# Kernel tuning notes

Hardware: AMD Instinct MI355X
Metric: run time of the kernel (lower is better)

Reference implementation:

```python
import jax, jax.numpy as jnp
import numpy as np

N_NODES = 100000
N_EDGES = 1600000
IN_F = 64
OUT_F = 32
NEG_SLOPE = 0.2


def setup_inputs() -> dict:
    key = jax.random.key(0)
    k = jax.random.split(key, 6)
    x = jax.random.normal(k[0], (N_NODES, IN_F), dtype=jnp.float32)
    edge_index = jax.random.randint(k[1], (2, N_EDGES), 0, N_NODES, dtype=jnp.int64)
    W = jax.random.normal(k[2], (IN_F, OUT_F), dtype=jnp.float32) * 0.1
    att_src = jax.random.normal(k[3], (OUT_F,), dtype=jnp.float32) * 0.1
    att_dst = jax.random.normal(k[4], (OUT_F,), dtype=jnp.float32) * 0.1
    bias = jax.random.normal(k[5], (OUT_F,), dtype=jnp.float32) * 0.1
    return {"x": x, "edge_index": edge_index, "W": W,
            "att_src": att_src, "att_dst": att_dst, "bias": bias}


def reference(x, edge_index, W, att_src, att_dst, bias):
    N = x.shape[0]
    # Linear projection (single head, concat=True -> [N, OUT_F])
    h = x @ W  # [N, C]
    a_src = h @ att_src  # [N] per-node source attention logit contribution
    a_dst = h @ att_dst  # [N] per-node destination contribution
    # add self loops (PyG GATConv default add_self_loops=True)
    loop = jnp.arange(N, dtype=edge_index.dtype)
    src = jnp.concatenate([edge_index[0], loop])  # [E+N] message senders
    dst = jnp.concatenate([edge_index[1], loop])  # [E+N] message receivers
    # attention logits per edge, LeakyReLU(alpha_src[j] + alpha_dst[i])
    e = jax.nn.leaky_relu(a_src[src] + a_dst[dst], NEG_SLOPE)
    # segment softmax over incoming edges of each destination node
    m = jax.ops.segment_max(e, dst, num_segments=N)  # every node has a self loop
    ex = jnp.exp(e - m[dst])
    denom = jax.ops.segment_sum(ex, dst, num_segments=N)
    alpha = ex / denom[dst]  # [E+N]
    # weighted scatter-add of source features into destinations
    out = jax.ops.segment_sum(h[src] * alpha[:, None], dst, num_segments=N)
    out = out + bias
    # GATLayer activation='relu'
    return jax.nn.relu(out)
```

## Files before the change

kernel.cpp:

```cpp
#include <hip/hip_runtime.h>
#include <hip/hip_fp16.h>
#include <math.h>

#define IN_F 64
#define OUT_F 32
#define NEG_SLOPE 0.2f

#define BK_SHIFT 7
#define BK 128
#define NBMAX 1024
#define NBLKA 256
#define PSTAGE 10
#define PADSLACK (BK * 15)

typedef _Float16 half8_t __attribute__((ext_vector_type(8)));
typedef float float4_t __attribute__((ext_vector_type(4)));
typedef int int4_t __attribute__((ext_vector_type(4)));


__device__ __forceinline__ float leaky(float v) {
    return (v > 0.0f) ? v : NEG_SLOPE * v;
}

__device__ __forceinline__ int incScan256(int v, int tid, int* wsum) {
    const int lane = tid & 63, wid = tid >> 6;
    #pragma unroll
    for (int m = 1; m < 64; m <<= 1) {
        int u = __shfl_up(v, m);
        if (lane >= m) v += u;
    }
    if (lane == 63) wsum[wid] = v;
    __syncthreads();
    int add = 0;
    for (int k = 0; k < wid; ++k) add += wsum[k];
    __syncthreads();
    return v + add;
}

__device__ __forceinline__ int incScan512(int v, int tid, int* wsum) {
    const int lane = tid & 63, wid = tid >> 6;
    #pragma unroll
    for (int m = 1; m < 64; m <<= 1) {
        int u = __shfl_up(v, m);
        if (lane >= m) v += u;
    }
    if (lane == 63) wsum[wid] = v;
    __syncthreads();
    int add = 0;
    for (int k = 0; k < wid; ++k) add += wsum[k];
    __syncthreads();
    return v + add;
}

__global__ __launch_bounds__(256) void k_projhist(
        const float* __restrict__ x, const float* __restrict__ W,
        const float* __restrict__ att_src, const float* __restrict__ att_dst,
        __half2* __restrict__ h2, float* __restrict__ asrc, float* __restrict__ adst,
        const int* __restrict__ dst, int* __restrict__ hist,
        int N, int NB, int E, int epb, int PB) {
    __shared__ int smem[2560];
    const int tid = threadIdx.x;

    if (blockIdx.x >= PB) {
        int* lh = smem;
        const int blk = blockIdx.x - PB;
        for (int i = tid; i < NB; i += 256) lh[i] = 0;
        __syncthreads();
        const int e0 = blk * epb, e1 = min(E, e0 + epb);
        for (int e = e0 + tid; e < e1; e += 256) atomicAdd(&lh[dst[e] >> BK_SHIFT], 1);
        __syncthreads();
        for (int b = tid; b < NB; b += 256) hist[(size_t)b * NBLKA + blk] = lh[b];
        return;
    }

    const int wv   = tid >> 6;
    const int lane = tid & 63;
    const int m    = lane & 15;
    const int quad = lane >> 4;
    const int node0 = (blockIdx.x * 4 + wv) * 16;
    if (node0 >= N) return;

    const int kb = quad * 8;
    half8_t b00, b01, b10, b11;
    #pragma unroll
    for (int j = 0; j < 8; ++j) {
        b00[j] = (_Float16)W[(kb + j) * OUT_F + m];
        b01[j] = (_Float16)W[(32 + kb + j) * OUT_F + m];
        b10[j] = (_Float16)W[(kb + j) * OUT_F + 16 + m];
        b11[j] = (_Float16)W[(32 + kb + j) * OUT_F + 16 + m];
    }
    const int row = min(node0 + m, N - 1);
    const float* xr = x + (size_t)row * IN_F + kb;
    float4_t xa = *(const float4_t*)(xr);
    float4_t xb = *(const float4_t*)(xr + 4);
    float4_t xc = *(const float4_t*)(xr + 32);
    float4_t xd = *(const float4_t*)(xr + 36);
    half8_t a0, a1;
    #pragma unroll
    for (int j = 0; j < 4; ++j) {
        a0[j] = (_Float16)xa[j]; a0[4 + j] = (_Float16)xb[j];
        a1[j] = (_Float16)xc[j]; a1[4 + j] = (_Float16)xd[j];
    }
    float4_t acc0 = {0.f, 0.f, 0.f, 0.f};
    float4_t acc1 = {0.f, 0.f, 0.f, 0.f};
    acc0 = __builtin_amdgcn_mfma_f32_16x16x32_f16(a0, b00, acc0, 0, 0, 0);
    acc0 = __builtin_amdgcn_mfma_f32_16x16x32_f16(a1, b01, acc0, 0, 0, 0);
    acc1 = __builtin_amdgcn_mfma_f32_16x16x32_f16(a0, b10, acc1, 0, 0, 0);
    acc1 = __builtin_amdgcn_mfma_f32_16x16x32_f16(a1, b11, acc1, 0, 0, 0);

    const float aS0 = att_src[m], aS1 = att_src[16 + m];
    const float aD0 = att_dst[m], aD1 = att_dst[16 + m];
    #pragma unroll
    for (int r = 0; r < 4; ++r) {
        const int node = node0 + quad * 4 + r;
        float h0 = acc0[r], h1 = acc1[r];
        float h0p = __shfl_xor(h0, 1);
        float h1p = __shfl_xor(h1, 1);
        if (node < N && (m & 1) == 0) {
            __half2 hv;
            hv.x = __float2half_rn(h0); hv.y = __float2half_rn(h0p);
            h2[(size_t)node * 16 + (m >> 1)] = hv;
            __half2 hw;
            hw.x = __float2half_rn(h1); hw.y = __float2half_rn(h1p);
            h2[(size_t)node * 16 + 8 + (m >> 1)] = hw;
        }
        float vs = h0 * aS0 + h1 * aS1;
        float vd = h0 * aD0 + h1 * aD1;
        #pragma unroll
        for (int mm = 1; mm < 16; mm <<= 1) {
            vs += __shfl_xor(vs, mm);
            vd += __shfl_xor(vd, mm);
        }
        if (node < N && m == 0) {
            asrc[node] = vs;
            adst[node] = vd;
        }
    }
}

__global__ __launch_bounds__(256) void k_scan1(int* __restrict__ hist,
                                               int* __restrict__ bsum,
                                               __half2* __restrict__ h2,
                                               float* __restrict__ asrc,
                                               int N, int NB) {
    __shared__ int wsum[4];
    const int b = blockIdx.x, tid = threadIdx.x;
    if (b == 0) {
        if (tid < 16) h2[(size_t)N * 16 + tid] = __floats2half2_rn(0.0f, 0.0f);
        if (tid == 16) asrc[N] = -1e30f;
    }
    int v = hist[(size_t)b * NBLKA + tid];
    const int inc = incScan256(v, tid, wsum);
    hist[(size_t)b * NBLKA + tid] = inc - v;
    if (tid == 255) bsum[b] = inc;
}

__global__ __launch_bounds__(512) void k_bpart(const int* __restrict__ src,
                                               const int* __restrict__ dst,
                                               const int* __restrict__ hist,
                                               const int* __restrict__ bsum,
                                               int* __restrict__ recs,
                                               int NB, int E, int epb) {
    __shared__ int tt[NBMAX];
    __shared__ int lcur[NBMAX];
    __shared__ int wsum[8];
    const int tid = threadIdx.x, blk = blockIdx.x;
    for (int i = tid; i < NBMAX; i += 512) tt[i] = (i < NB) ? bsum[i] : 0;
    __syncthreads();
    {
        int a0 = tt[tid * 2], a1 = tt[tid * 2 + 1];
        int s = a0 + a1;
        int inc = incScan512(s, tid, wsum);
        int run = inc - s;
        tt[tid * 2] = run; run += a0;
        tt[tid * 2 + 1] = run;
    }
    __syncthreads();
    for (int b = tid; b < NB; b += 512)
        lcur[b] = hist[(size_t)b * NBLKA + blk] + tt[b];
    __syncthreads();
    const int e0 = blk * epb, e1 = min(E, e0 + epb);
    for (int e = e0 + tid; e < e1; e += 512) {
        int s = src[e];
        int d = dst[e];
        int p = atomicAdd(&lcur[d >> BK_SHIFT], 1);
        recs[p] = ((d & (BK - 1)) << 17) | s;
    }
}

__global__ __launch_bounds__(256) void k_place(const int* __restrict__ recs,
                                               const int* __restrict__ bsum,
                                               int* __restrict__ cnt,
                                               int* __restrict__ offs,
                                               int* __restrict__ col,
                                               int NB, int E, int N) {
    __shared__ int tt[NBMAX];
    __shared__ int fineCnt[BK];
    __shared__ int cur[BK];
    __shared__ int wsum[4];
    const int b = blockIdx.x, tid = threadIdx.x;
    for (int i = tid; i < NBMAX; i += 256) tt[i] = (i < NB) ? bsum[i] : 0;
    __syncthreads();
    {
        int a0 = tt[tid * 4], a1 = tt[tid * 4 + 1], a2 = tt[tid * 4 + 2], a3 = tt[tid * 4 + 3];
        int s = a0 + a1 + a2 + a3;
        int inc = incScan256(s, tid, wsum);
        int run = inc - s;
        tt[tid * 4] = run;     run += a0;
        tt[tid * 4 + 1] = run; run += a1;
        tt[tid * 4 + 2] = run; run += a2;
        tt[tid * 4 + 3] = run;
    }
    __syncthreads();
    const int cb0 = tt[b];
    const int cb1 = (b + 1 < NB) ? tt[b + 1] : E;
    const int count = cb1 - cb0;
    const int colBase = cb0 + b * PADSLACK;
    for (int i = tid; i < count + PADSLACK; i += 256) col[colBase + i] = N;
    int myrec[PSTAGE];
    if (tid < BK) fineCnt[tid] = 0;
    __syncthreads();
    #pragma unroll
    for (int k = 0; k < PSTAGE; ++k) {
        int i = tid + k * 256;
        if (i < count) {
            int v = recs[cb0 + i];
            myrec[k] = v;
            atomicAdd(&fineCnt[v >> 17], 1);
        }
    }
    for (int i = tid + PSTAGE * 256; i < count; i += 256)
        atomicAdd(&fineCnt[recs[cb0 + i] >> 17], 1);
    __syncthreads();
    const int v0 = (tid < BK) ? fineCnt[tid] : 0;
    const int pv = (v0 + 15) & ~15;
    const int pinc = incScan256(pv, tid, wsum);
    const int pexcl = pinc - pv;
    if (tid < BK) {
        const int node = (b << BK_SHIFT) + tid;
        if (node < N) {
            cnt[node]  = pv;
            offs[node] = colBase + pexcl;
        }
        cur[tid] = colBase + pexcl;
    }
    __syncthreads();
    #pragma unroll
    for (int k = 0; k < PSTAGE; ++k) {
        int i = tid + k * 256;
        if (i < count) {
            int r = myrec[k];
            int p = atomicAdd(&cur[r >> 17], 1);
            col[p] = r & 0x1FFFF;
        }
    }
    for (int i = tid + PSTAGE * 256; i < count; i += 256) {
        int r = recs[cb0 + i];
        int p = atomicAdd(&cur[r >> 17], 1);
        col[p] = r & 0x1FFFF;
    }
}

__global__ void k_gather(const int* __restrict__ col, const int* __restrict__ offs,
                         const int* __restrict__ cnt, const float* __restrict__ asrc,
                         const float* __restrict__ adst, const __half2* __restrict__ h2,
                         const float* __restrict__ bias, float* __restrict__ out, int N) {
    int t = blockIdx.x * 256 + threadIdx.x;
    int n = t >> 6;
    if (n >= N) return;
    const int lane = t & 63;
    const int g  = lane >> 4;
    const int c2 = lane & 15;
    const float adst_n = adst[n];
    float l = 0.0f, accx = 0.0f, accy = 0.0f;
    if (g == 0) {
        float p = __expf(leaky(asrc[n] + adst_n));
        float2 hv = __half22float2(h2[(size_t)n * 16 + c2]);
        l = p; accx = p * hv.x; accy = p * hv.y;
    }
    const int off = offs[n];
    const int q = cnt[n] >> 2;
    const int j0 = off + g * q;
    const int jend = j0 + q;
    for (int j = j0; j < jend; j += 4) {
        int s0 = col[j], s1 = col[j + 1], s2 = col[j + 2], s3 = col[j + 3];
        float a0 = asrc[s0], a1 = asrc[s1], a2 = asrc[s2], a3 = asrc[s3];
        float2 h0 = __half22float2(h2[(size_t)s0 * 16 + c2]);
        float2 h1 = __half22float2(h2[(size_t)s1 * 16 + c2]);
        float2 hv2 = __half22float2(h2[(size_t)s2 * 16 + c2]);
        float2 h3 = __half22float2(h2[(size_t)s3 * 16 + c2]);
        float p0 = __expf(leaky(a0 + adst_n));
        float p1 = __expf(leaky(a1 + adst_n));
        float p2 = __expf(leaky(a2 + adst_n));
        float p3 = __expf(leaky(a3 + adst_n));
        l += (p0 + p1) + (p2 + p3);
        accx += p0 * h0.x + p1 * h1.x + p2 * hv2.x + p3 * h3.x;
        accy += p0 * h0.y + p1 * h1.y + p2 * hv2.y + p3 * h3.y;
    }
    l    += __shfl_xor(l, 16);    l    += __shfl_xor(l, 32);
    accx += __shfl_xor(accx, 16); accx += __shfl_xor(accx, 32);
    accy += __shfl_xor(accy, 16); accy += __shfl_xor(accy, 32);
    if (g == 0) {
        float inv = 1.0f / l;
        float2 bb = ((const float2*)bias)[c2];
        float2 o;
        o.x = fmaxf(accx * inv + bb.x, 0.0f);
        o.y = fmaxf(accy * inv + bb.y, 0.0f);
        ((float2*)out)[(size_t)n * 16 + c2] = o;
    }
}

extern "C" void kernel_launch(void* const* d_in, const int* in_sizes, int n_in,
                              void* d_out, int out_size, void* d_ws, size_t ws_size,
                              hipStream_t stream) {
    const float* x        = (const float*)d_in[0];
    const int*   eidx     = (const int*)d_in[1];
    const float* W        = (const float*)d_in[2];
    const float* att_src  = (const float*)d_in[3];
    const float* att_dst  = (const float*)d_in[4];
    const float* bias     = (const float*)d_in[5];
    float* out = (float*)d_out;

    const int N = in_sizes[0] / IN_F;
    const int E = in_sizes[1] / 2;
    const int* src = eidx;
    const int* dst = eidx + E;

    const int NB  = (N + BK - 1) >> BK_SHIFT;
    const int epb = (E + NBLKA - 1) / NBLKA;

    int* u = (int*)d_ws;
    size_t o = 0;
    __half2* h2   = (__half2*)(u + o); o += (size_t)(N + 1) * 16;
    float*   asrc = (float*)(u + o);   o += N + 1;
    float*   adst = (float*)(u + o);   o += N;
    int*     cnt  = u + o;             o += N;
    int*     offs = u + o;             o += N;
    int*     hist = u + o;             o += (size_t)NB * NBLKA;
    int*     bsum = u + o;             o += NBMAX;
    int*     col  = u + o;             o += (size_t)E + (size_t)NB * PADSLACK;
    int*     recs = u + o;             o += E;

    const int PB = (N + 63) / 64;
    const int gatherBlocks = ((size_t)N * 64 + 255) / 256;

    k_projhist<<<PB + NBLKA, 256, 0, stream>>>(x, W, att_src, att_dst, h2, asrc, adst,
                                               dst, hist, N, NB, E, epb, PB);
    k_scan1<<<NB, 256, 0, stream>>>(hist, bsum, h2, asrc, N, NB);
    k_bpart<<<NBLKA, 512, 0, stream>>>(src, dst, hist, bsum, recs, NB, E, epb);
    k_place<<<NB, 256, 0, stream>>>(recs, bsum, cnt, offs, col, NB, E, N);
    k_gather<<<gatherBlocks, 256, 0, stream>>>(col, offs, cnt, asrc, adst, h2, bias, out, N);
}
```

Before: 175.0 us.

## Fuse CSR placement and gather into one kernel with LDS-resident column lists

Merges the k_place and k_gather kernels. Each 128-node bucket block now sorts its edge records into a shared-memory column array and computes its nodes' softmax-weighted aggregation directly from LDS. This removes the global col/offs/cnt writes and reads, one kernel launch, and the larger 16-entry per-node padding, which is now 4. The trade-offs are a fixed LDS capacity of 4096 entries per bucket that fails on skewed graphs, and only NB blocks of 512 threads doing the gather, which may reduce parallelism compared with one wavefront per node.

```diff
diff --git a/kernel.cpp b/kernel.cpp
--- a/kernel.cpp
+++ b/kernel.cpp
@@ -10,8 +10,8 @@
 #define BK 128
 #define NBMAX 1024
 #define NBLKA 256
-#define PSTAGE 10
-#define PADSLACK (BK * 15)
+#define PSTAGE 5
+#define COLCAP 4096
 
 typedef _Float16 half8_t __attribute__((ext_vector_type(8)));
 typedef float float4_t __attribute__((ext_vector_type(4)));
@@ -188,125 +188,129 @@
     }
 }
 
-__global__ __launch_bounds__(256) void k_place(const int* __restrict__ recs,
-                                               const int* __restrict__ bsum,
-                                               int* __restrict__ cnt,
-                                               int* __restrict__ offs,
-                                               int* __restrict__ col,
-                                               int NB, int E, int N) {
+__global__ __launch_bounds__(512) void k_pg(const int* __restrict__ recs,
+                                            const int* __restrict__ bsum,
+                                            const float* __restrict__ asrc,
+                                            const float* __restrict__ adst,
+                                            const __half2* __restrict__ h2,
+                                            const float* __restrict__ bias,
+                                            float* __restrict__ out,
+                                            int NB, int E, int N) {
     __shared__ int tt[NBMAX];
+    __shared__ __align__(16) int colsh[COLCAP];
     __shared__ int fineCnt[BK];
     __shared__ int cur[BK];
-    __shared__ int wsum[4];
+    __shared__ int loff[BK];
+    __shared__ int lpad[BK];
+    __shared__ int wsum[8];
     const int b = blockIdx.x, tid = threadIdx.x;
-    for (int i = tid; i < NBMAX; i += 256) tt[i] = (i < NB) ? bsum[i] : 0;
+    const int node0 = b << BK_SHIFT;
+
+    for (int i = tid; i < NBMAX; i += 512) tt[i] = (i < NB) ? bsum[i] : 0;
     __syncthreads();
     {
-        int a0 = tt[tid * 4], a1 = tt[tid * 4 + 1], a2 = tt[tid * 4 + 2], a3 = tt[tid * 4 + 3];
-        int s = a0 + a1 + a2 + a3;
-        int inc = incScan256(s, tid, wsum);
+        int a0 = tt[tid * 2], a1 = tt[tid * 2 + 1];
+        int s = a0 + a1;
+        int inc = incScan512(s, tid, wsum);
         int run = inc - s;
-        tt[tid * 4] = run;     run += a0;
-        tt[tid * 4 + 1] = run; run += a1;
-        tt[tid * 4 + 2] = run; run += a2;
-        tt[tid * 4 + 3] = run;
+        tt[tid * 2] = run;
+        tt[tid * 2 + 1] = run + a0;
     }
     __syncthreads();
     const int cb0 = tt[b];
     const int cb1 = (b + 1 < NB) ? tt[b + 1] : E;
     const int count = cb1 - cb0;
-    const int colBase = cb0 + b * PADSLACK;
-    for (int i = tid; i < count + PADSLACK; i += 256) col[colBase + i] = N;
+
+    for (int i = tid; i < COLCAP; i += 512) colsh[i] = N;
+    if (tid < BK) fineCnt[tid] = 0;
+    __syncthreads();
+
     int myrec[PSTAGE];
-    if (tid < BK) fineCnt[tid] = 0;
-    __syncthreads();
     #pragma unroll
     for (int k = 0; k < PSTAGE; ++k) {
-        int i = tid + k * 256;
+        int i = tid + k * 512;
         if (i < count) {
             int v = recs[cb0 + i];
             myrec[k] = v;
             atomicAdd(&fineCnt[v >> 17], 1);
         }
     }
-    for (int i = tid + PSTAGE * 256; i < count; i += 256)
+    for (int i = tid + PSTAGE * 512; i < count; i += 512)
         atomicAdd(&fineCnt[recs[cb0 + i] >> 17], 1);
     __syncthreads();
+
     const int v0 = (tid < BK) ? fineCnt[tid] : 0;
-    const int pv = (v0 + 15) & ~15;
-    const int pinc = incScan256(pv, tid, wsum);
-    const int pexcl = pinc - pv;
+    const int pv = (v0 + 3) & ~3;
+    const int vin = (tid < BK) ? pv : 0;
+    const int pinc = incScan512(vin, tid, wsum);
+    const int pexcl = pinc - vin;
     if (tid < BK) {
-        const int node = (b << BK_SHIFT) + tid;
-        if (node < N) {
-            cnt[node]  = pv;
-            offs[node] = colBase + pexcl;
-        }
-        cur[tid] = colBase + pexcl;
-    }
-    __syncthreads();
+        loff[tid] = pexcl;
+        lpad[tid] = pv;
+        cur[tid]  = pexcl;
+    }
+    __syncthreads();
+
     #pragma unroll
     for (int k = 0; k < PSTAGE; ++k) {
-        int i = tid + k * 256;
+        int i = tid + k * 512;
         if (i < count) {
             int r = myrec[k];
             int p = atomicAdd(&cur[r >> 17], 1);
-            col[p] = r & 0x1FFFF;
-        }
-    }
-    for (int i = tid + PSTAGE * 256; i < count; i += 256) {
+            colsh[p] = r & 0x1FFFF;
+        }
+    }
+    for (int i = tid + PSTAGE * 512; i < count; i += 512) {
         int r = recs[cb0 + i];
         int p = atomicAdd(&cur[r >> 17], 1);
-        col[p] = r & 0x1FFFF;
-    }
-}
-
-__global__ void k_gather(const int* __restrict__ col, const int* __restrict__ offs,
-                         const int* __restrict__ cnt, const float* __restrict__ asrc,
-                         const float* __restrict__ adst, const __half2* __restrict__ h2,
-                         const float* __restrict__ bias, float* __restrict__ out, int N) {
-    int t = blockIdx.x * 256 + threadIdx.x;
-    int n = t >> 6;
-    if (n >= N) return;
-    const int lane = t & 63;
-    const int g  = lane >> 4;
-    const int c2 = lane & 15;
-    const float adst_n = adst[n];
-    float l = 0.0f, accx = 0.0f, accy = 0.0f;
-    if (g == 0) {
-        float p = __expf(leaky(asrc[n] + adst_n));
-        float2 hv = __half22float2(h2[(size_t)n * 16 + c2]);
-        l = p; accx = p * hv.x; accy = p * hv.y;
-    }
-    const int off = offs[n];
-    const int q = cnt[n] >> 2;
-    const int j0 = off + g * q;
-    const int jend = j0 + q;
-    for (int j = j0; j < jend; j += 4) {
-        int s0 = col[j], s1 = col[j + 1], s2 = col[j + 2], s3 = col[j + 3];
-        float a0 = asrc[s0], a1 = asrc[s1], a2 = asrc[s2], a3 = asrc[s3];
-        float2 h0 = __half22float2(h2[(size_t)s0 * 16 + c2]);
-        float2 h1 = __half22float2(h2[(size_t)s1 * 16 + c2]);
-        float2 hv2 = __half22float2(h2[(size_t)s2 * 16 + c2]);
-        float2 h3 = __half22float2(h2[(size_t)s3 * 16 + c2]);
-        float p0 = __expf(leaky(a0 + adst_n));
-        float p1 = __expf(leaky(a1 + adst_n));
-        float p2 = __expf(leaky(a2 + adst_n));
-        float p3 = __expf(leaky(a3 + adst_n));
-        l += (p0 + p1) + (p2 + p3);
-        accx += p0 * h0.x + p1 * h1.x + p2 * hv2.x + p3 * h3.x;
-        accy += p0 * h0.y + p1 * h1.y + p2 * hv2.y + p3 * h3.y;
-    }
-    l    += __shfl_xor(l, 16);    l    += __shfl_xor(l, 32);
-    accx += __shfl_xor(accx, 16); accx += __shfl_xor(accx, 32);
-    accy += __shfl_xor(accy, 16); accy += __shfl_xor(accy, 32);
-    if (g == 0) {
-        float inv = 1.0f / l;
-        float2 bb = ((const float2*)bias)[c2];
-        float2 o;
-        o.x = fmaxf(accx * inv + bb.x, 0.0f);
-        o.y = fmaxf(accy * inv + bb.y, 0.0f);
-        ((float2*)out)[(size_t)n * 16 + c2] = o;
+        colsh[p] = r & 0x1FFFF;
+    }
+    __syncthreads();
+
+    const int wid  = tid >> 6;
+    const int lane = tid & 63;
+    const int g    = lane >> 4;
+    const int c2   = lane & 15;
+    for (int i = 0; i < 16; ++i) {
+        const int dloc = wid * 16 + i;
+        const int n = node0 + dloc;
+        if (n >= N) break;
+        const float adst_n = adst[n];
+        float l = 0.0f, accx = 0.0f, accy = 0.0f;
+        if (g == 0) {
+            float p = __expf(leaky(asrc[n] + adst_n));
+            float2 hv = __half22float2(h2[(size_t)n * 16 + c2]);
+            l = p; accx = p * hv.x; accy = p * hv.y;
+        }
+        const int base = loff[dloc];
+        const int nch  = lpad[dloc] >> 2;
+        for (int c = g; c < nch; c += 4) {
+            const int4_t cc = *(const int4_t*)(&colsh[base + c * 4]);
+            const int s0 = cc[0], s1 = cc[1], s2 = cc[2], s3 = cc[3];
+            float a0 = asrc[s0], a1 = asrc[s1], a2 = asrc[s2], a3 = asrc[s3];
+            float2 h0 = __half22float2(h2[(size_t)s0 * 16 + c2]);
+            float2 h1 = __half22float2(h2[(size_t)s1 * 16 + c2]);
+            float2 hv2 = __half22float2(h2[(size_t)s2 * 16 + c2]);
+            float2 h3 = __half22float2(h2[(size_t)s3 * 16 + c2]);
+            float p0 = __expf(leaky(a0 + adst_n));
+            float p1 = __expf(leaky(a1 + adst_n));
+            float p2 = __expf(leaky(a2 + adst_n));
+            float p3 = __expf(leaky(a3 + adst_n));
+            l += (p0 + p1) + (p2 + p3);
+            accx += p0 * h0.x + p1 * h1.x + p2 * hv2.x + p3 * h3.x;
+            accy += p0 * h0.y + p1 * h1.y + p2 * hv2.y + p3 * h3.y;
+        }
+        l    += __shfl_xor(l, 16);    l    += __shfl_xor(l, 32);
+        accx += __shfl_xor(accx, 16); accx += __shfl_xor(accx, 32);
+        accy += __shfl_xor(accy, 16); accy += __shfl_xor(accy, 32);
+        if (g == 0) {
+            float inv = 1.0f / l;
+            float2 bb = ((const float2*)bias)[c2];
+            float2 o;
+            o.x = fmaxf(accx * inv + bb.x, 0.0f);
+            o.y = fmaxf(accy * inv + bb.y, 0.0f);
+            ((float2*)out)[(size_t)n * 16 + c2] = o;
+        }
     }
 }
 
@@ -334,20 +338,15 @@
     __half2* h2   = (__half2*)(u + o); o += (size_t)(N + 1) * 16;
     float*   asrc = (float*)(u + o);   o += N + 1;
     float*   adst = (float*)(u + o);   o += N;
-    int*     cnt  = u + o;             o += N;
-    int*     offs = u + o;             o += N;
     int*     hist = u + o;             o += (size_t)NB * NBLKA;
     int*     bsum = u + o;             o += NBMAX;
-    int*     col  = u + o;             o += (size_t)E + (size_t)NB * PADSLACK;
     int*     recs = u + o;             o += E;
 
     const int PB = (N + 63) / 64;
-    const int gatherBlocks = ((size_t)N * 64 + 255) / 256;
 
     k_projhist<<<PB + NBLKA, 256, 0, stream>>>(x, W, att_src, att_dst, h2, asrc, adst,
                                                dst, hist, N, NB, E, epb, PB);
     k_scan1<<<NB, 256, 0, stream>>>(hist, bsum, h2, asrc, N, NB);
     k_bpart<<<NBLKA, 512, 0, stream>>>(src, dst, hist, bsum, recs, NB, E, epb);
-    k_place<<<NB, 256, 0, stream>>>(recs, bsum, cnt, offs, col, NB, E, N);
-    k_gather<<<gatherBlocks, 256, 0, stream>>>(col, offs, cnt, asrc, adst, h2, bias, out, N);
-}
+    k_pg<<<NB, 512, 0, stream>>>(recs, bsum, asrc, adst, h2, bias, out, NB, E, N);
+}
```

Measured after the change: 158.5 us. 1.1x faster.
